# Kernel optimization log

Measured on AMD Instinct MI355X. Metric: run time of the kernel, lower is better.

## Reference

```python
import jax, jax.numpy as jnp
import numpy as np

N, D, F = 10000, 32, 512  # nodes, fixed in-degree, in_feats == out_feats


def _lstm_last(mail, Wih, Whh, bih, bhh):
    """Run a PyTorch-convention LSTM over mailbox [N, D, F_in]; return final hidden [N, H].
    Gate order i, f, g, o; zero initial state (matches DGL's lstm reducer and h_final usage)."""
    n, _, _ = mail.shape
    H = Whh.shape[1]
    h0 = jnp.zeros((n, H), mail.dtype)
    c0 = jnp.zeros((n, H), mail.dtype)

    def step(carry, xt):  # xt: [N, F_in]
        h, c = carry
        g = xt @ Wih.T + bih + h @ Whh.T + bhh  # [N, 4H]
        i, f, gg, o = jnp.split(g, 4, axis=-1)
        c = jax.nn.sigmoid(f) * c + jax.nn.sigmoid(i) * jnp.tanh(gg)
        h = jax.nn.sigmoid(o) * jnp.tanh(c)
        return (h, c), None

    (hT, _), _ = jax.lax.scan(step, (h0, c0), jnp.swapaxes(mail, 0, 1))
    return hT


def setup_inputs() -> dict:
    key = jax.random.key(0)
    ks = jax.random.split(key, 12)
    s = 1.0 / np.sqrt(F)
    inp = {
        "x": jax.random.normal(ks[0], (N, F), jnp.float32),
        "src": jax.random.randint(ks[1], (N, D), 0, N),
        # SAGEConv internal LSTM (hidden = in_feats)
        "Wih1": jax.random.uniform(ks[2], (4 * F, F), jnp.float32, -s, s),
        "Whh1": jax.random.uniform(ks[3], (4 * F, F), jnp.float32, -s, s),
        "bih1": jnp.zeros((4 * F,), jnp.float32),
        "bhh1": jnp.zeros((4 * F,), jnp.float32),
        # SAGEConv linear layers
        "W_self": jax.random.normal(ks[4], (F, F), jnp.float32) * s,
        "W_neigh": jax.random.normal(ks[5], (F, F), jnp.float32) * s,
        "b": jnp.zeros((F,), jnp.float32),
        # outer LSTM (self.lstm): input in_feats, hidden out_feats
        "Wih2": jax.random.uniform(ks[6], (4 * F, F), jnp.float32, -s, s),
        "Whh2": jax.random.uniform(ks[7], (4 * F, F), jnp.float32, -s, s),
        "bih2": jnp.zeros((4 * F,), jnp.float32),
        "bhh2": jnp.zeros((4 * F,), jnp.float32),
    }
    return inp


def reference(x, src, Wih1, Whh1, bih1, bhh1, W_self, W_neigh, b, Wih2, Whh2, bih2, bhh2):
    # Stage 1: SAGEConv with lstm aggregator (eval mode, feat_drop identity)
    mail1 = x[src]                                  # [N, D, F] neighbor mailbox
    h_neigh = _lstm_last(mail1, Wih1, Whh1, bih1, bhh1)  # [N, F]
    h = x @ W_self + h_neigh @ W_neigh + b          # [N, F]
    # Stage 2: custom reduce — per-node LSTM over mailbox of stage-1 outputs
    mail2 = h[src]                                  # [N, D, F]
    out = _lstm_last(mail2, Wih2, Whh2, bih2, bhh2)  # [N, F]
    return out
```

## Files before the change

kernel.cpp:

```cpp
#include <hip/hip_runtime.h>

#define NROWS 10000
#define DDEG  32
#define FDIM  512
#define MP    10112
#define MT    79
#define GN    2048
#define MTILE 48
#define NBLK  209

typedef unsigned short u16;
typedef __bf16 bf16x8 __attribute__((ext_vector_type(8)));
typedef float  float4v __attribute__((ext_vector_type(4)));
typedef _Float16 half4 __attribute__((ext_vector_type(4)));

typedef __attribute__((address_space(3))) uint32_t lds_u32;
typedef __attribute__((address_space(1))) const uint32_t gbl_u32;

__device__ __forceinline__ void load_lds16(const void* g, void* l) {
    __builtin_amdgcn_global_load_lds((gbl_u32*)g, (lds_u32*)l, 16, 0, 0);
}

__device__ __forceinline__ u16 f2b(float f) {
    union { unsigned u; float f; } v; v.f = f;
    unsigned u = v.u;
    return (u16)((u + 0x7fffu + ((u >> 16) & 1u)) >> 16);
}
__device__ __forceinline__ float sigm(float x) { return 1.f / (1.f + __expf(-x)); }
__device__ __forceinline__ float tanh_fast(float x) {
    float e = __expf(2.f * x);
    return 1.f - 2.f / (e + 1.f);
}

__device__ __forceinline__ float4v mfma16(bf16x8 a, bf16x8 b, float4v c) {
    return __builtin_amdgcn_mfma_f32_16x16x32_bf16(a, b, c, 0, 0, 0);
}

__device__ __forceinline__ void gemm_core(const u16* __restrict__ A, const u16* __restrict__ B,
                                          int K, int mB, int nB,
                                          u16* Asm, u16* Bsm, float4v acc[4][4])
{
    const int tid  = threadIdx.x;
    const int lane = tid & 63, wid = tid >> 6;
    const int wm = (wid >> 1) << 6, wn = (wid & 1) << 6;
    const int l15 = lane & 15, quad = lane >> 4;
    const int ktn = K >> 5;
    for (int kt = 0; kt < ktn; ++kt) {
        __syncthreads();
        const int kof = kt << 5;
#pragma unroll
        for (int it = 0; it < 2; ++it) {
            int c   = (it << 8) + (wid << 6) + lane;
            int row = c >> 2, kc = c & 3;
            int ldsbase = ((it << 8) + (wid << 6)) << 3;
            load_lds16(A + (size_t)(mB + row) * 512 + kof + (kc << 3), &Asm[ldsbase]);
            load_lds16(B + (size_t)(nB + row) * 512 + kof + (kc << 3), &Bsm[ldsbase]);
        }
        __syncthreads();
        bf16x8 af[4], bfr[4];
#pragma unroll
        for (int i = 0; i < 4; ++i) {
            af[i]  = *(const bf16x8*)(void*)&Asm[(wm + (i << 4) + l15) * 32 + quad * 8];
            bfr[i] = *(const bf16x8*)(void*)&Bsm[(wn + (i << 4) + l15) * 32 + quad * 8];
        }
#pragma unroll
        for (int mi = 0; mi < 4; ++mi)
#pragma unroll
            for (int ni = 0; ni < 4; ++ni)
                acc[mi][ni] = mfma16(af[mi], bfr[ni], acc[mi][ni]);
    }
}

__global__ void __launch_bounds__(256)
gemm_gatex(const u16* __restrict__ A, const u16* __restrict__ B,
           const float4v* __restrict__ biasv, half4* __restrict__ gX)
{
    __shared__ u16 Asm[128 * 32], Bsm[128 * 32];
    const int mB = blockIdx.x << 7, nB = blockIdx.y << 7;
    const int tid = threadIdx.x, lane = tid & 63, wid = tid >> 6;
    const int wm = (wid >> 1) << 6, wn = (wid & 1) << 6;
    const int l15 = lane & 15, quad = lane >> 4;
    float4v acc[4][4];
    float4v z = {0.f, 0.f, 0.f, 0.f};
#pragma unroll
    for (int i = 0; i < 4; ++i)
#pragma unroll
        for (int j = 0; j < 4; ++j) acc[i][j] = z;
    gemm_core(A, B, 512, mB, nB, Asm, Bsm, acc);
    const int slab = nB + wn;
    const int unit = ((slab >> 6) << 4) + l15;
    float4v b4 = biasv[unit];
#pragma unroll
    for (int mi = 0; mi < 4; ++mi) {
        int m0 = mB + wm + (mi << 4) + (quad << 2);
#pragma unroll
        for (int r = 0; r < 4; ++r) {
            int m = m0 + r;
            if (m < NROWS) {
                half4 o;
                o[0] = (_Float16)(acc[mi][0][r] + b4[0]);
                o[1] = (_Float16)(acc[mi][1][r] + b4[1]);
                o[2] = (_Float16)(acc[mi][2][r] + b4[2]);
                o[3] = (_Float16)(acc[mi][3][r] + b4[3]);
                gX[(size_t)m * 512 + unit] = o;
            }
        }
    }
}

__global__ void __launch_bounds__(256)
gemm_sage(const u16* __restrict__ A1, const u16* __restrict__ B1,
          const u16* __restrict__ A2, const u16* __restrict__ B2,
          const float* __restrict__ bias, u16* __restrict__ C)
{
    __shared__ u16 Asm[128 * 32], Bsm[128 * 32];
    const int mB = blockIdx.x << 7, nB = blockIdx.y << 7;
    const int tid = threadIdx.x, lane = tid & 63, wid = tid >> 6;
    const int wm = (wid >> 1) << 6, wn = (wid & 1) << 6;
    const int l15 = lane & 15, quad = lane >> 4;
    float4v acc[4][4];
    float4v z = {0.f, 0.f, 0.f, 0.f};
#pragma unroll
    for (int i = 0; i < 4; ++i)
#pragma unroll
        for (int j = 0; j < 4; ++j) acc[i][j] = z;
    gemm_core(A1, B1, 512, mB, nB, Asm, Bsm, acc);
    gemm_core(A2, B2, 512, mB, nB, Asm, Bsm, acc);
#pragma unroll
    for (int mi = 0; mi < 4; ++mi) {
        int m0 = mB + wm + (mi << 4) + (quad << 2);
#pragma unroll
        for (int ni = 0; ni < 4; ++ni) {
            int n = nB + wn + (ni << 4) + l15;
            float bb = bias[n];
#pragma unroll
            for (int r = 0; r < 4; ++r) {
                int m = m0 + r;
                if (m < NROWS) C[(size_t)m * 512 + n] = f2b(acc[mi][ni][r] + bb);
            }
        }
    }
}

__global__ void __launch_bounds__(512, 2)
lstm_scan(const u16* __restrict__ Bf, const half4* __restrict__ gX,
          const int* __restrict__ src, u16* __restrict__ hf_bf16, float* __restrict__ out_f32)
{
    __shared__ u16 hbuf[2][MTILE][520];
    __shared__ int srcl[MTILE * DDEG];
    const int tid = threadIdx.x;
    const int w = tid >> 6, lane = tid & 63;
    const int l15 = lane & 15, quad = lane >> 4;
    const int m0 = blockIdx.x * MTILE;

    {
        uint32_t* hz = (uint32_t*)&hbuf[0][0][0];
        for (int i = tid; i < MTILE * 520 / 2; i += 512) hz[i] = 0u;
    }
    for (int i = tid; i < MTILE * DDEG; i += 512) {
        int g = m0 * DDEG + i;
        srcl[i] = (g < NROWS * DDEG) ? src[g] : 0;
    }
    __syncthreads();

    float cst[4][12];
#pragma unroll
    for (int p = 0; p < 4; ++p)
#pragma unroll
        for (int i = 0; i < 12; ++i) cst[p][i] = 0.f;

    for (int t = 0; t < DDEG; ++t) {
        const u16(*hc)[520] = hbuf[t & 1];
        u16(*hn)[520] = hbuf[(t + 1) & 1];
#pragma unroll
        for (int p = 0; p < 4; ++p) {
            const int grp = (w << 2) + p;
            const int unit = (grp << 4) + l15;
            half4 gv[12];
#pragma unroll
            for (int mi = 0; mi < 3; ++mi)
#pragma unroll
                for (int r = 0; r < 4; ++r) {
                    int ml = (mi << 4) + (quad << 2) + r;
                    int s = srcl[ml * DDEG + t];
                    gv[mi * 4 + r] = gX[(size_t)s * 512 + unit];
                }
            float4v acc[3][4];
            float4v z = {0.f, 0.f, 0.f, 0.f};
#pragma unroll
            for (int mi = 0; mi < 3; ++mi)
#pragma unroll
                for (int g = 0; g < 4; ++g) acc[mi][g] = z;
#pragma unroll 4
            for (int kt = 0; kt < 16; ++kt) {
                bf16x8 af[3], bfr[4];
#pragma unroll
                for (int mi = 0; mi < 3; ++mi)
                    af[mi] = *(const bf16x8*)(void*)&hc[(mi << 4) + l15][(kt << 5) + (quad << 3)];
                const u16* bp = Bf + (((grp << 4) + kt) << 11) + (lane << 3);
#pragma unroll
                for (int s_ = 0; s_ < 4; ++s_)
                    bfr[s_] = *(const bf16x8*)(void*)(bp + (s_ << 9));
#pragma unroll
                for (int mi = 0; mi < 3; ++mi)
#pragma unroll
                    for (int g = 0; g < 4; ++g)
                        acc[mi][g] = mfma16(af[mi], bfr[g], acc[mi][g]);
            }
#pragma unroll
            for (int mi = 0; mi < 3; ++mi)
#pragma unroll
                for (int r = 0; r < 4; ++r) {
                    int idx = mi * 4 + r;
                    int ml = (mi << 4) + (quad << 2) + r;
                    float gi = acc[mi][0][r] + (float)gv[idx][0];
                    float gf = acc[mi][1][r] + (float)gv[idx][1];
                    float gg = acc[mi][2][r] + (float)gv[idx][2];
                    float go = acc[mi][3][r] + (float)gv[idx][3];
                    float cn = sigm(gf) * cst[p][idx] + sigm(gi) * tanh_fast(gg);
                    cst[p][idx] = cn;
                    float hv = sigm(go) * tanh_fast(cn);
                    hn[ml][unit] = f2b(hv);
                    if (t == DDEG - 1) {
                        int m = m0 + ml;
                        if (m < NROWS) {
                            if (hf_bf16) hf_bf16[(size_t)m * 512 + unit] = f2b(hv);
                            if (out_f32) out_f32[(size_t)m * 512 + unit] = hv;
                        }
                    }
                }
        }
        __syncthreads();
    }
}

__global__ void prep_lstm_w(const float* __restrict__ Wih,
                            const float* __restrict__ bih, const float* __restrict__ bhh,
                            u16* __restrict__ Wih_p, float* __restrict__ biasv)
{
    int idx = blockIdx.x * 256 + threadIdx.x;
    int p = idx >> 9, k = idx & 511;
    int gate = (p >> 4) & 3, grp = p >> 6, u = p & 15;
    int srow = (gate << 9) + (grp << 4) + u;
    Wih_p[idx] = f2b(Wih[(srow << 9) + k]);
    if (k == 0) {
        int unit = (grp << 4) + u;
        biasv[(unit << 2) + gate] = bih[srow] + bhh[srow];
    }
}

__global__ void prep_whh_frag(const float* __restrict__ Whh, u16* __restrict__ Bf)
{
    int chunk = blockIdx.x * 256 + threadIdx.x;
    int lane = chunk & 63, s_ = (chunk >> 6) & 3, kt = (chunk >> 8) & 15, grp = chunk >> 12;
    int srow = (s_ << 9) + (grp << 4) + (lane & 15);
    int k0 = (kt << 5) + ((lane >> 4) << 3);
    const float* srcp = Whh + (srow << 9) + k0;
    u16* dst = Bf + (chunk << 3);
#pragma unroll
    for (int j = 0; j < 8; ++j) dst[j] = f2b(srcp[j]);
}

__global__ void prep_misc(const float* __restrict__ Wself, const float* __restrict__ Wneigh,
                          const float* __restrict__ x,
                          u16* __restrict__ WselfT, u16* __restrict__ WneighT,
                          u16* __restrict__ xp)
{
    int idx = blockIdx.x * 256 + threadIdx.x;
    if (idx < 512 * 512) {
        int n = idx >> 9, k = idx & 511;
        WselfT[idx]  = f2b(Wself[(k << 9) + n]);
        WneighT[idx] = f2b(Wneigh[(k << 9) + n]);
    }
    xp[idx] = (idx < NROWS * 512) ? f2b(x[idx]) : (u16)0;
}

extern "C" void kernel_launch(void* const* d_in, const int* in_sizes, int n_in,
                              void* d_out, int out_size, void* d_ws, size_t ws_size,
                              hipStream_t stream) {
    (void)in_sizes; (void)n_in; (void)out_size; (void)ws_size;
    const float* x     = (const float*)d_in[0];
    const int*   src   = (const int*)d_in[1];
    const float* Wih1  = (const float*)d_in[2];
    const float* Whh1  = (const float*)d_in[3];
    const float* bih1  = (const float*)d_in[4];
    const float* bhh1  = (const float*)d_in[5];
    const float* Wself = (const float*)d_in[6];
    const float* Wneigh= (const float*)d_in[7];
    const float* bvec  = (const float*)d_in[8];
    const float* Wih2  = (const float*)d_in[9];
    const float* Whh2  = (const float*)d_in[10];
    const float* bih2  = (const float*)d_in[11];
    const float* bhh2  = (const float*)d_in[12];
    float* out = (float*)d_out;

    char* w = (char*)d_ws;
    auto alloc = [&](size_t bytes) { char* p = w; w += (bytes + 255) & ~(size_t)255; return p; };
    u16*   xp     = (u16*)  alloc((size_t)MP * 512 * 2);
    u16*   ha     = (u16*)  alloc((size_t)MP * 512 * 2);
    u16*   hs     = (u16*)  alloc((size_t)MP * 512 * 2);
    half4* gateX  = (half4*)alloc((size_t)NROWS * 512 * 8);
    u16*   Wih1p  = (u16*)  alloc((size_t)GN * 512 * 2);
    u16*   Wih2p  = (u16*)  alloc((size_t)GN * 512 * 2);
    u16*   Bf1    = (u16*)  alloc((size_t)GN * 512 * 2);
    u16*   Bf2    = (u16*)  alloc((size_t)GN * 512 * 2);
    u16*   WselfT = (u16*)  alloc((size_t)512 * 512 * 2);
    u16*   WneighT= (u16*)  alloc((size_t)512 * 512 * 2);
    float* biasv1 = (float*)alloc(GN * 4);
    float* biasv2 = (float*)alloc(GN * 4);

    dim3 blk(256);
    prep_lstm_w<<<4096, blk, 0, stream>>>(Wih1, bih1, bhh1, Wih1p, biasv1);
    prep_lstm_w<<<4096, blk, 0, stream>>>(Wih2, bih2, bhh2, Wih2p, biasv2);
    prep_whh_frag<<<512, blk, 0, stream>>>(Whh1, Bf1);
    prep_whh_frag<<<512, blk, 0, stream>>>(Whh2, Bf2);
    prep_misc<<<20224, blk, 0, stream>>>(Wself, Wneigh, x, WselfT, WneighT, xp);

    gemm_gatex<<<dim3(MT, 16), blk, 0, stream>>>(xp, Wih1p, (const float4v*)biasv1, gateX);
    lstm_scan<<<NBLK, 512, 0, stream>>>(Bf1, gateX, src, ha, nullptr);
    gemm_sage<<<dim3(MT, 4), blk, 0, stream>>>(xp, WselfT, ha, WneighT, bvec, hs);
    gemm_gatex<<<dim3(MT, 16), blk, 0, stream>>>(hs, Wih2p, (const float4v*)biasv2, gateX);
    lstm_scan<<<NBLK, 512, 0, stream>>>(Bf2, gateX, src, nullptr, out);
}
```

Measured before the change: 2.698 ms.

## Split LSTM scan by hidden slices with register-resident Whh and inter-block barriers

The LSTM recurrence kernel is restructured so each block owns a slice of hidden units for a 320-row tile and keeps its recurrent-weight fragments in registers instead of re-reading them from global memory every step. Hidden state is exchanged through global ping-pong buffers loaded asynchronously into LDS, and blocks in the same row tile synchronise each timestep with an atomic counter spin barrier. The aim is to remove repeated Whh traffic and raise parallelism. In exchange it adds a grid-wide dependency that requires all 256 blocks to be co-resident, plus extra global round-trips for h and cell state kept in LDS.

```diff
diff --git a/kernel.cpp b/kernel.cpp
--- a/kernel.cpp
+++ b/kernel.cpp
@@ -6,8 +6,8 @@
 #define MP    10112
 #define MT    79
 #define GN    2048
-#define MTILE 48
-#define NBLK  209
+#define MROWS 10240
+#define ASTR  536
 
 typedef unsigned short u16;
 typedef __bf16 bf16x8 __attribute__((ext_vector_type(8)));
@@ -31,7 +31,6 @@
     float e = __expf(2.f * x);
     return 1.f - 2.f / (e + 1.f);
 }
-
 __device__ __forceinline__ float4v mfma16(bf16x8 a, bf16x8 b, float4v c) {
     return __builtin_amdgcn_mfma_f32_16x16x32_bf16(a, b, c, 0, 0, 0);
 }
@@ -143,94 +142,117 @@
 }
 
 __global__ void __launch_bounds__(512, 2)
-lstm_scan(const u16* __restrict__ Bf, const half4* __restrict__ gX,
-          const int* __restrict__ src, u16* __restrict__ hf_bf16, float* __restrict__ out_f32)
-{
-    __shared__ u16 hbuf[2][MTILE][520];
-    __shared__ int srcl[MTILE * DDEG];
-    const int tid = threadIdx.x;
-    const int w = tid >> 6, lane = tid & 63;
-    const int l15 = lane & 15, quad = lane >> 4;
-    const int m0 = blockIdx.x * MTILE;
-
+lstm_scanB(const u16* __restrict__ Bf, const half4* __restrict__ gX,
+           const int* __restrict__ src, u16* __restrict__ h0buf, u16* __restrict__ h1buf,
+           int* __restrict__ ctr, float* __restrict__ out_f32)
+{
+    __shared__ u16 Asm[2][32][ASTR];
+    __shared__ float cs[320 * 64];
+    const int tid = threadIdx.x, w = tid >> 6, lane = tid & 63;
+    const int l15 = lane & 15, quad = lane >> 4, v = l15 & 7, hi = l15 >> 3;
+    const int mt = blockIdx.x & 31, sl = blockIdx.x >> 5;
+    const int G = sl * 8 + w, unit = G * 8 + v;
+    const int m0 = mt * 320;
+
+    bf16x8 Breg[2][16];
     {
-        uint32_t* hz = (uint32_t*)&hbuf[0][0][0];
-        for (int i = tid; i < MTILE * 520 / 2; i += 512) hz[i] = 0u;
-    }
-    for (int i = tid; i < MTILE * DDEG; i += 512) {
-        int g = m0 * DDEG + i;
-        srcl[i] = (g < NROWS * DDEG) ? src[g] : 0;
-    }
+        const u16* bgp = Bf + ((size_t)G << 14) + (lane << 3);
+#pragma unroll
+        for (int tile = 0; tile < 2; ++tile)
+#pragma unroll
+            for (int kt = 0; kt < 16; ++kt)
+                Breg[tile][kt] = *(const bf16x8*)(void*)(bgp + (tile << 13) + (kt << 9));
+    }
+    for (int i = tid; i < 320 * 64; i += 512) cs[i] = 0.f;
     __syncthreads();
 
-    float cst[4][12];
-#pragma unroll
-    for (int p = 0; p < 4; ++p)
-#pragma unroll
-        for (int i = 0; i < 12; ++i) cst[p][i] = 0.f;
-
+    u16* bufs[2] = {h0buf, h1buf};
     for (int t = 0; t < DDEG; ++t) {
-        const u16(*hc)[520] = hbuf[t & 1];
-        u16(*hn)[520] = hbuf[(t + 1) & 1];
-#pragma unroll
-        for (int p = 0; p < 4; ++p) {
-            const int grp = (w << 2) + p;
-            const int unit = (grp << 4) + l15;
-            half4 gv[12];
-#pragma unroll
-            for (int mi = 0; mi < 3; ++mi)
+        const u16* hsrc = bufs[t & 1];
+        u16* hdst = bufs[(t + 1) & 1];
+        if (t > 0) {
+#pragma unroll
+            for (int rr = 0; rr < 4; ++rr) {
+                int row = (w << 2) + rr;
+                load_lds16(hsrc + (size_t)(m0 + row) * 512 + (lane << 3),
+                           &Asm[0][row][0] + (lane << 3));
+            }
+        }
+        for (int c = 0; c < 10; ++c) {
+            const int mbase = m0 + (c << 5);
+            if (t > 0) {
+                __syncthreads();
+                if (c < 9) {
+#pragma unroll
+                    for (int rr = 0; rr < 4; ++rr) {
+                        int row = (w << 2) + rr;
+                        load_lds16(hsrc + (size_t)(mbase + 32 + row) * 512 + (lane << 3),
+                                   &Asm[(c + 1) & 1][row][0] + (lane << 3));
+                    }
+                }
+            }
+            half4 gv[8];
+#pragma unroll
+            for (int mi = 0; mi < 2; ++mi)
 #pragma unroll
                 for (int r = 0; r < 4; ++r) {
-                    int ml = (mi << 4) + (quad << 2) + r;
-                    int s = srcl[ml * DDEG + t];
+                    int m = mbase + (mi << 4) + (quad << 2) + r;
+                    int s = (m < NROWS) ? src[m * DDEG + t] : 0;
                     gv[mi * 4 + r] = gX[(size_t)s * 512 + unit];
                 }
-            float4v acc[3][4];
+            float4v acc[2][2];
             float4v z = {0.f, 0.f, 0.f, 0.f};
-#pragma unroll
-            for (int mi = 0; mi < 3; ++mi)
-#pragma unroll
-                for (int g = 0; g < 4; ++g) acc[mi][g] = z;
-#pragma unroll 4
-            for (int kt = 0; kt < 16; ++kt) {
-                bf16x8 af[3], bfr[4];
-#pragma unroll
-                for (int mi = 0; mi < 3; ++mi)
-                    af[mi] = *(const bf16x8*)(void*)&hc[(mi << 4) + l15][(kt << 5) + (quad << 3)];
-                const u16* bp = Bf + (((grp << 4) + kt) << 11) + (lane << 3);
-#pragma unroll
-                for (int s_ = 0; s_ < 4; ++s_)
-                    bfr[s_] = *(const bf16x8*)(void*)(bp + (s_ << 9));
-#pragma unroll
-                for (int mi = 0; mi < 3; ++mi)
-#pragma unroll
-                    for (int g = 0; g < 4; ++g)
-                        acc[mi][g] = mfma16(af[mi], bfr[g], acc[mi][g]);
-            }
-#pragma unroll
-            for (int mi = 0; mi < 3; ++mi)
+            acc[0][0] = z; acc[0][1] = z; acc[1][0] = z; acc[1][1] = z;
+            if (t > 0) {
+                const u16* ab = &Asm[c & 1][0][0];
+#pragma unroll
+                for (int kt = 0; kt < 16; ++kt) {
+                    bf16x8 a0 = *(const bf16x8*)(void*)(ab + l15 * ASTR + (kt << 5) + (quad << 3));
+                    bf16x8 a1 = *(const bf16x8*)(void*)(ab + (16 + l15) * ASTR + (kt << 5) + (quad << 3));
+                    acc[0][0] = mfma16(a0, Breg[0][kt], acc[0][0]);
+                    acc[0][1] = mfma16(a0, Breg[1][kt], acc[0][1]);
+                    acc[1][0] = mfma16(a1, Breg[0][kt], acc[1][0]);
+                    acc[1][1] = mfma16(a1, Breg[1][kt], acc[1][1]);
+                }
+            }
+#pragma unroll
+            for (int mi = 0; mi < 2; ++mi)
 #pragma unroll
                 for (int r = 0; r < 4; ++r) {
-                    int idx = mi * 4 + r;
+                    float t0 = acc[mi][0][r], t1 = acc[mi][1][r];
+                    float p0 = __shfl_xor(t0, 8, 64);
+                    float p1 = __shfl_xor(t1, 8, 64);
                     int ml = (mi << 4) + (quad << 2) + r;
-                    float gi = acc[mi][0][r] + (float)gv[idx][0];
-                    float gf = acc[mi][1][r] + (float)gv[idx][1];
-                    float gg = acc[mi][2][r] + (float)gv[idx][2];
-                    float go = acc[mi][3][r] + (float)gv[idx][3];
-                    float cn = sigm(gf) * cst[p][idx] + sigm(gi) * tanh_fast(gg);
-                    cst[p][idx] = cn;
-                    float hv = sigm(go) * tanh_fast(cn);
-                    hn[ml][unit] = f2b(hv);
-                    if (t == DDEG - 1) {
-                        int m = m0 + ml;
-                        if (m < NROWS) {
-                            if (hf_bf16) hf_bf16[(size_t)m * 512 + unit] = f2b(hv);
-                            if (out_f32) out_f32[(size_t)m * 512 + unit] = hv;
-                        }
+                    int m = mbase + ml;
+                    half4 g4 = gv[mi * 4 + r];
+                    float gi_ = t0 + (float)g4[0];
+                    float gf_ = p0 + (float)g4[1];
+                    float gg_ = t1 + (float)g4[2];
+                    float go_ = p1 + (float)g4[3];
+                    if (hi == 0) {
+                        int ci = (((c << 5) + ml) << 6) + (w << 3) + v;
+                        float cn = sigm(gf_) * cs[ci] + sigm(gi_) * tanh_fast(gg_);
+                        cs[ci] = cn;
+                        float hv = sigm(go_) * tanh_fast(cn);
+                        hdst[(size_t)m * 512 + unit] = f2b(hv);
+                        if (out_f32 && t == DDEG - 1 && m < NROWS)
+                            out_f32[(size_t)m * 512 + unit] = hv;
                     }
                 }
         }
-        __syncthreads();
+        if (t < DDEG - 1) {
+            __threadfence();
+            __syncthreads();
+            if (tid == 0) {
+                atomicAdd(&ctr[mt], 1);
+                int target = 8 * (t + 1);
+                while (__hip_atomic_load(&ctr[mt], __ATOMIC_ACQUIRE,
+                                         __HIP_MEMORY_SCOPE_AGENT) < target)
+                    __builtin_amdgcn_s_sleep(2);
+            }
+            __syncthreads();
+            __threadfence();
+        }
     }
 }
 
@@ -249,16 +271,19 @@
     }
 }
 
-__global__ void prep_whh_frag(const float* __restrict__ Whh, u16* __restrict__ Bf)
-{
-    int chunk = blockIdx.x * 256 + threadIdx.x;
-    int lane = chunk & 63, s_ = (chunk >> 6) & 3, kt = (chunk >> 8) & 15, grp = chunk >> 12;
-    int srow = (s_ << 9) + (grp << 4) + (lane & 15);
-    int k0 = (kt << 5) + ((lane >> 4) << 3);
-    const float* srcp = Whh + (srow << 9) + k0;
-    u16* dst = Bf + (chunk << 3);
-#pragma unroll
-    for (int j = 0; j < 8; ++j) dst[j] = f2b(srcp[j]);
+__global__ void prep_whhB(const float* __restrict__ Whh, u16* __restrict__ Bf)
+{
+    int thr = blockIdx.x * 256 + threadIdx.x;
+    int lane = thr & 63, kt = (thr >> 6) & 15, tile = (thr >> 10) & 1, G = thr >> 11;
+    int l15 = lane & 15, quad = lane >> 4;
+    int colin = (tile << 4) + l15;
+    int gate = colin >> 3, v = colin & 7;
+    int srow = (gate << 9) + (G << 3) + v;
+    int k0 = (kt << 5) + (quad << 3);
+    const float* sp = Whh + ((size_t)srow << 9) + k0;
+    u16* dp = Bf + ((size_t)thr << 3);
+#pragma unroll
+    for (int j = 0; j < 8; ++j) dp[j] = f2b(sp[j]);
 }
 
 __global__ void prep_misc(const float* __restrict__ Wself, const float* __restrict__ Wneigh,
@@ -274,6 +299,8 @@
     }
     xp[idx] = (idx < NROWS * 512) ? f2b(x[idx]) : (u16)0;
 }
+
+__global__ void zero_ctr(int* __restrict__ ctr) { ctr[threadIdx.x] = 0; }
 
 extern "C" void kernel_launch(void* const* d_in, const int* in_sizes, int n_in,
                               void* d_out, int out_size, void* d_ws, size_t ws_size,
@@ -297,7 +324,8 @@
     char* w = (char*)d_ws;
     auto alloc = [&](size_t bytes) { char* p = w; w += (bytes + 255) & ~(size_t)255; return p; };
     u16*   xp     = (u16*)  alloc((size_t)MP * 512 * 2);
-    u16*   ha     = (u16*)  alloc((size_t)MP * 512 * 2);
+    u16*   hA     = (u16*)  alloc((size_t)MROWS * 512 * 2);
+    u16*   hB     = (u16*)  alloc((size_t)MROWS * 512 * 2);
     u16*   hs     = (u16*)  alloc((size_t)MP * 512 * 2);
     half4* gateX  = (half4*)alloc((size_t)NROWS * 512 * 8);
     u16*   Wih1p  = (u16*)  alloc((size_t)GN * 512 * 2);
@@ -308,17 +336,19 @@
     u16*   WneighT= (u16*)  alloc((size_t)512 * 512 * 2);
     float* biasv1 = (float*)alloc(GN * 4);
     float* biasv2 = (float*)alloc(GN * 4);
+    int*   ctrs   = (int*)  alloc(64 * 4);
 
     dim3 blk(256);
     prep_lstm_w<<<4096, blk, 0, stream>>>(Wih1, bih1, bhh1, Wih1p, biasv1);
     prep_lstm_w<<<4096, blk, 0, stream>>>(Wih2, bih2, bhh2, Wih2p, biasv2);
-    prep_whh_frag<<<512, blk, 0, stream>>>(Whh1, Bf1);
-    prep_whh_frag<<<512, blk, 0, stream>>>(Whh2, Bf2);
+    prep_whhB<<<512, blk, 0, stream>>>(Whh1, Bf1);
+    prep_whhB<<<512, blk, 0, stream>>>(Whh2, Bf2);
     prep_misc<<<20224, blk, 0, stream>>>(Wself, Wneigh, x, WselfT, WneighT, xp);
+    zero_ctr<<<1, 64, 0, stream>>>(ctrs);
 
     gemm_gatex<<<dim3(MT, 16), blk, 0, stream>>>(xp, Wih1p, (const float4v*)biasv1, gateX);
-    lstm_scan<<<NBLK, 512, 0, stream>>>(Bf1, gateX, src, ha, nullptr);
-    gemm_sage<<<dim3(MT, 4), blk, 0, stream>>>(xp, WselfT, ha, WneighT, bvec, hs);
+    lstm_scanB<<<256, 512, 0, stream>>>(Bf1, gateX, src, hA, hB, ctrs, nullptr);
+    gemm_sage<<<dim3(MT, 4), blk, 0, stream>>>(xp, WselfT, hA, WneighT, bvec, hs);
     gemm_gatex<<<dim3(MT, 16), blk, 0, stream>>>(hs, Wih2p, (const float4v*)biasv2, gateX);
-    lstm_scan<<<NBLK, 512, 0, stream>>>(Bf2, gateX, src, nullptr, out);
-}
+    lstm_scanB<<<256, 512, 0, stream>>>(Bf2, gateX, src, hA, hB, ctrs + 32, out);
+}
```

After: 10.14 ms. +276.0%, slower.
